# Performance work log

Measured on AMD Instinct MI355X. Metric: run time of the kernel, lower is better.

The kernel has to match this reference:

```python
import jax, jax.numpy as jnp
import numpy as np

N_ENTITY = 500000
N_RELATION = 1000
EMB = 128
BATCH = 131072


def setup_inputs() -> dict:
    key = jax.random.key(0)
    k_h, k_r, k_t, k_e, k_rel = jax.random.split(key, 5)
    head = jax.random.randint(k_h, (BATCH,), 0, N_ENTITY)
    rel = jax.random.randint(k_r, (BATCH,), 0, N_RELATION)
    tail = jax.random.randint(k_t, (BATCH,), 0, N_ENTITY)
    triple = jnp.stack([head, rel, tail], axis=1)  # [B,3] int
    # init_weights: uniform(-0.1, 0.1) for embeddings
    entity_emb = jax.random.uniform(k_e, (N_ENTITY, EMB), jnp.float32, -0.1, 0.1)
    relation_emb = jax.random.uniform(k_rel, (N_RELATION, EMB), jnp.float32, -0.1, 0.1)
    De = jnp.eye(EMB, dtype=jnp.float32)
    Dr = jnp.eye(EMB, dtype=jnp.float32)
    b_c = jnp.zeros((BATCH, EMB), dtype=jnp.float32)
    return {"triple": triple, "entity_emb": entity_emb, "relation_emb": relation_emb,
            "De": De, "Dr": Dr, "b_c": b_c}


def reference(triple, entity_emb, relation_emb, De, Dr, b_c):
    # flag == 0 path (default): combine head+relation, score against tail
    h = entity_emb[triple[:, 0]]        # [B,E] gather
    r = relation_emb[triple[:, 1]]      # [B,E] gather
    t = entity_emb[triple[:, 2]]        # [B,E] gather
    f = jnp.tanh(h @ De + r @ Dr + b_c)  # [B,E]
    score = jnp.sum(f * t, axis=1, keepdims=True)  # vectorized per-row dot -> [B,1]
    return jax.nn.sigmoid(score)
```

## Files before the change

### kernel.cpp

```cpp
#include <hip/hip_runtime.h>

#define EMB 128
#define BM 128
#define THREADS 512

typedef __attribute__((ext_vector_type(8))) short bf16x8;
typedef __attribute__((ext_vector_type(4))) float f32x4;
typedef unsigned short u16;

__device__ __forceinline__ u16 f2bf(float f) {
    unsigned u = __builtin_bit_cast(unsigned, f);
    u += 0x7fffu + ((u >> 16) & 1u);
    return (u16)(u >> 16);
}

__global__ void relproj_kernel(const float* __restrict__ rel,
                               const float* __restrict__ Dr,
                               float* __restrict__ Rp, int nrel) {
    const int n  = threadIdx.x;
    const int j0 = blockIdx.x * 4;
    if (j0 >= nrel) return;
    float a0 = 0.f, a1 = 0.f, a2 = 0.f, a3 = 0.f;
    for (int k = 0; k < EMB; ++k) {
        const float dr = Dr[k * EMB + n];
        a0 = fmaf(rel[(j0 + 0) * EMB + k], dr, a0);
        a1 = fmaf(rel[(j0 + 1) * EMB + k], dr, a1);
        a2 = fmaf(rel[(j0 + 2) * EMB + k], dr, a2);
        a3 = fmaf(rel[(j0 + 3) * EMB + k], dr, a3);
    }
    Rp[(j0 + 0) * EMB + n] = a0;
    Rp[(j0 + 1) * EMB + n] = a1;
    Rp[(j0 + 2) * EMB + n] = a2;
    Rp[(j0 + 3) * EMB + n] = a3;
}

__global__ void bimg_kernel(const float* __restrict__ De, u16* __restrict__ Bimg) {
    const int idx  = blockIdx.x * 256 + threadIdx.x;
    const int e    = idx & 7;
    const int lane = (idx >> 3) & 63;
    const int frag = idx >> 9;
    const int ni = frag & 7, kk = frag >> 3;
    const int k = kk * 32 + (lane >> 4) * 8 + e;
    const int n = ni * 16 + (lane & 15);
    Bimg[idx] = f2bf(De[k * EMB + n]);
}

__global__ __launch_bounds__(THREADS, 4)
void projE_main(const int* __restrict__ triple,
                const float* __restrict__ ent,
                const float* __restrict__ bc,
                const float* __restrict__ Rp,
                const u16* __restrict__ Bimg,
                float* __restrict__ out)
{
    __shared__ u16 As[BM][EMB];
    __shared__ u16 Bs[16384];

    const int tid  = threadIdx.x;
    const int lane = tid & 63;
    const int w    = tid >> 6;
    const int l15  = lane & 15;
    const int l4   = lane >> 4;
    const int bm0  = blockIdx.x * BM;

    {
        const __attribute__((address_space(1))) char* gB =
            (const __attribute__((address_space(1))) char*)Bimg;
        __attribute__((address_space(3))) char* lB =
            (__attribute__((address_space(3))) char*)Bs;
        #pragma unroll
        for (int i = 0; i < 4; ++i) {
            const int off = (i * THREADS + tid) * 16;
            __builtin_amdgcn_global_load_lds(
                (const __attribute__((address_space(1))) void*)(gB + off),
                (__attribute__((address_space(3))) void*)(lB + off), 16, 0, 0);
        }
    }

    {
        const int seg   = lane & 31;
        const int rhalf = lane >> 5;
        #pragma unroll
        for (int it = 0; it < 8; ++it) {
            const int row  = w * 16 + it * 2 + rhalf;
            const int g    = bm0 + row;
            const int hidx = triple[g * 3];
            const float4 hv = *reinterpret_cast<const float4*>(ent + (size_t)hidx * EMB + seg * 4);
            ushort4 hp = { f2bf(hv.x), f2bf(hv.y), f2bf(hv.z), f2bf(hv.w) };
            *reinterpret_cast<ushort4*>(&As[row][(seg * 4) ^ ((row & 7) << 3)]) = hp;
        }
    }

    __syncthreads();

    f32x4 acc[8];
    #pragma unroll
    for (int ni = 0; ni < 8; ++ni) acc[ni] = (f32x4){0.f, 0.f, 0.f, 0.f};

    const int arow = w * 16 + l15;
    const int asw  = (arow & 7) << 3;
    #pragma unroll
    for (int kk = 0; kk < 4; ++kk) {
        const bf16x8 a = *reinterpret_cast<const bf16x8*>(&As[arow][(kk * 32 + 8 * l4) ^ asw]);
        #pragma unroll
        for (int ni = 0; ni < 8; ++ni) {
            const bf16x8 b = *reinterpret_cast<const bf16x8*>(&Bs[(kk * 8 + ni) * 512 + lane * 8]);
            acc[ni] = __builtin_amdgcn_mfma_f32_16x16x32_bf16(a, b, acc[ni], 0, 0, 0);
        }
    }

    #pragma unroll
    for (int r = 0; r < 4; ++r) {
        const int row  = w * 16 + 4 * l4 + r;
        const int g    = bm0 + row;
        const int ridx = triple[g * 3 + 1];
        const int tidx = triple[g * 3 + 2];
        const float* rp = Rp  + (size_t)ridx * EMB;
        const float* bp = bc  + (size_t)g    * EMB;
        const float* tp = ent + (size_t)tidx * EMB;
        float dot = 0.f;
        #pragma unroll
        for (int ni = 0; ni < 8; ++ni) {
            const int col = ni * 16 + l15;
            const float x  = acc[ni][r] + rp[col] + bp[col];
            const float e2 = __expf(2.f * x);
            const float fv = 1.f - __fdividef(2.f, e2 + 1.f);
            dot = fmaf(fv, tp[col], dot);
        }
        dot += __shfl_xor(dot, 1);
        dot += __shfl_xor(dot, 2);
        dot += __shfl_xor(dot, 4);
        dot += __shfl_xor(dot, 8);
        if (l15 == 0) out[g] = __fdividef(1.f, 1.f + __expf(-dot));
    }
}

extern "C" void kernel_launch(void* const* d_in, const int* in_sizes, int n_in,
                              void* d_out, int out_size, void* d_ws, size_t ws_size,
                              hipStream_t stream) {
    const int*   triple = (const int*)  d_in[0];
    const float* ent    = (const float*)d_in[1];
    const float* rel    = (const float*)d_in[2];
    const float* De     = (const float*)d_in[3];
    const float* Dr     = (const float*)d_in[4];
    const float* bc     = (const float*)d_in[5];
    float* out = (float*)d_out;

    const int batch = in_sizes[0] / 3;
    const int nrel  = in_sizes[2] / EMB;

    float* Rp = (float*)d_ws;
    u16* Bimg = (u16*)((char*)d_ws + 524288);

    relproj_kernel<<<dim3((nrel + 3) / 4), dim3(EMB), 0, stream>>>(rel, Dr, Rp, nrel);
    bimg_kernel<<<dim3(64), dim3(256), 0, stream>>>(De, Bimg);
    projE_main<<<dim3(batch / BM), dim3(THREADS), 0, stream>>>(triple, ent, bc, Rp, Bimg, out);
}
```

Baseline: 45.33 us.

## Transpose MFMA operands for row-contiguous epilogue and merge setup kernels

Swaps the A/B operands of the MFMA so each lane's accumulator holds four consecutive columns of one row. The epilogue can then use float4 loads of the relation projection, bias and tail rows, and a two-step shuffle reduction replaces the four-step one. The relation-projection and De-conversion kernels are merged into a single setup launch, which removes one kernel launch. The hardcoded 500-block split assumes nrel ≤ 1000.

```diff
diff --git a/kernel.cpp b/kernel.cpp
--- a/kernel.cpp
+++ b/kernel.cpp
@@ -14,35 +14,30 @@
     return (u16)(u >> 16);
 }
 
-__global__ void relproj_kernel(const float* __restrict__ rel,
-                               const float* __restrict__ Dr,
-                               float* __restrict__ Rp, int nrel) {
-    const int n  = threadIdx.x;
-    const int j0 = blockIdx.x * 4;
-    if (j0 >= nrel) return;
-    float a0 = 0.f, a1 = 0.f, a2 = 0.f, a3 = 0.f;
-    for (int k = 0; k < EMB; ++k) {
-        const float dr = Dr[k * EMB + n];
-        a0 = fmaf(rel[(j0 + 0) * EMB + k], dr, a0);
-        a1 = fmaf(rel[(j0 + 1) * EMB + k], dr, a1);
-        a2 = fmaf(rel[(j0 + 2) * EMB + k], dr, a2);
-        a3 = fmaf(rel[(j0 + 3) * EMB + k], dr, a3);
+__global__ void setup_kernel(const float* __restrict__ rel,
+                             const float* __restrict__ Dr,
+                             const float* __restrict__ De,
+                             float* __restrict__ Rp,
+                             u16* __restrict__ Bimg, int nrel) {
+    const int blk = blockIdx.x;
+    if (blk < 500) {
+        const int n = threadIdx.x & 127;
+        const int j = blk * 2 + (threadIdx.x >> 7);
+        if (j >= nrel) return;
+        float a = 0.f;
+        for (int k = 0; k < EMB; ++k)
+            a = fmaf(rel[(size_t)j * EMB + k], Dr[(size_t)k * EMB + n], a);
+        Rp[(size_t)j * EMB + n] = a;
+    } else {
+        const int idx  = (blk - 500) * 256 + threadIdx.x;
+        const int e    = idx & 7;
+        const int lane = (idx >> 3) & 63;
+        const int frag = idx >> 9;
+        const int ni = frag & 7, kk = frag >> 3;
+        const int k = kk * 32 + (lane >> 4) * 8 + e;
+        const int n = ni * 16 + (lane & 15);
+        Bimg[idx] = f2bf(De[(size_t)k * EMB + n]);
     }
-    Rp[(j0 + 0) * EMB + n] = a0;
-    Rp[(j0 + 1) * EMB + n] = a1;
-    Rp[(j0 + 2) * EMB + n] = a2;
-    Rp[(j0 + 3) * EMB + n] = a3;
-}
-
-__global__ void bimg_kernel(const float* __restrict__ De, u16* __restrict__ Bimg) {
-    const int idx  = blockIdx.x * 256 + threadIdx.x;
-    const int e    = idx & 7;
-    const int lane = (idx >> 3) & 63;
-    const int frag = idx >> 9;
-    const int ni = frag & 7, kk = frag >> 3;
-    const int k = kk * 32 + (lane >> 4) * 8 + e;
-    const int n = ni * 16 + (lane & 15);
-    Bimg[idx] = f2bf(De[k * EMB + n]);
 }
 
 __global__ __launch_bounds__(THREADS, 4)
@@ -95,44 +90,45 @@
 
     f32x4 acc[8];
     #pragma unroll
-    for (int ni = 0; ni < 8; ++ni) acc[ni] = (f32x4){0.f, 0.f, 0.f, 0.f};
+    for (int ci = 0; ci < 8; ++ci) acc[ci] = (f32x4){0.f, 0.f, 0.f, 0.f};
 
     const int arow = w * 16 + l15;
     const int asw  = (arow & 7) << 3;
     #pragma unroll
     for (int kk = 0; kk < 4; ++kk) {
-        const bf16x8 a = *reinterpret_cast<const bf16x8*>(&As[arow][(kk * 32 + 8 * l4) ^ asw]);
+        const bf16x8 h = *reinterpret_cast<const bf16x8*>(&As[arow][(kk * 32 + 8 * l4) ^ asw]);
         #pragma unroll
-        for (int ni = 0; ni < 8; ++ni) {
-            const bf16x8 b = *reinterpret_cast<const bf16x8*>(&Bs[(kk * 8 + ni) * 512 + lane * 8]);
-            acc[ni] = __builtin_amdgcn_mfma_f32_16x16x32_bf16(a, b, acc[ni], 0, 0, 0);
+        for (int ci = 0; ci < 8; ++ci) {
+            const bf16x8 d = *reinterpret_cast<const bf16x8*>(&Bs[(kk * 8 + ci) * 512 + lane * 8]);
+            acc[ci] = __builtin_amdgcn_mfma_f32_16x16x32_bf16(d, h, acc[ci], 0, 0, 0);
         }
     }
 
+    const int g    = bm0 + w * 16 + l15;
+    const int ridx = triple[g * 3 + 1];
+    const int tidx = triple[g * 3 + 2];
+    const float* rp = Rp  + (size_t)ridx * EMB;
+    const float* bp = bc  + (size_t)g    * EMB;
+    const float* tp = ent + (size_t)tidx * EMB;
+
+    float dot = 0.f;
     #pragma unroll
-    for (int r = 0; r < 4; ++r) {
-        const int row  = w * 16 + 4 * l4 + r;
-        const int g    = bm0 + row;
-        const int ridx = triple[g * 3 + 1];
-        const int tidx = triple[g * 3 + 2];
-        const float* rp = Rp  + (size_t)ridx * EMB;
-        const float* bp = bc  + (size_t)g    * EMB;
-        const float* tp = ent + (size_t)tidx * EMB;
-        float dot = 0.f;
+    for (int ci = 0; ci < 8; ++ci) {
+        const int col = ci * 16 + 4 * l4;
+        const float4 r4 = *reinterpret_cast<const float4*>(rp + col);
+        const float4 b4 = *reinterpret_cast<const float4*>(bp + col);
+        const float4 t4 = *reinterpret_cast<const float4*>(tp + col);
         #pragma unroll
-        for (int ni = 0; ni < 8; ++ni) {
-            const int col = ni * 16 + l15;
-            const float x  = acc[ni][r] + rp[col] + bp[col];
+        for (int e = 0; e < 4; ++e) {
+            const float x  = acc[ci][e] + (&r4.x)[e] + (&b4.x)[e];
             const float e2 = __expf(2.f * x);
             const float fv = 1.f - __fdividef(2.f, e2 + 1.f);
-            dot = fmaf(fv, tp[col], dot);
+            dot = fmaf(fv, (&t4.x)[e], dot);
         }
-        dot += __shfl_xor(dot, 1);
-        dot += __shfl_xor(dot, 2);
-        dot += __shfl_xor(dot, 4);
-        dot += __shfl_xor(dot, 8);
-        if (l15 == 0) out[g] = __fdividef(1.f, 1.f + __expf(-dot));
     }
+    dot += __shfl_xor(dot, 16);
+    dot += __shfl_xor(dot, 32);
+    if (lane < 16) out[g] = __fdividef(1.f, 1.f + __expf(-dot));
 }
 
 extern "C" void kernel_launch(void* const* d_in, const int* in_sizes, int n_in,
@@ -152,7 +148,6 @@
     float* Rp = (float*)d_ws;
     u16* Bimg = (u16*)((char*)d_ws + 524288);
 
-    relproj_kernel<<<dim3((nrel + 3) / 4), dim3(EMB), 0, stream>>>(rel, Dr, Rp, nrel);
-    bimg_kernel<<<dim3(64), dim3(256), 0, stream>>>(De, Bimg);
+    setup_kernel<<<dim3(564), dim3(256), 0, stream>>>(rel, Dr, De, Rp, Bimg, nrel);
     projE_main<<<dim3(batch / BM), dim3(THREADS), 0, stream>>>(triple, ent, bc, Rp, Bimg, out);
 }
```

New measurement: 46.04 us. About the same (+1.6%).
